# Performance work log

Measured on AMD Instinct MI355X. Metric: run time of the kernel, lower is better.

Reference implementation:

```python
import jax, jax.numpy as jnp
import numpy as np

D_MODEL, N_STATE, L_MAX, BATCH = 512, 64, 2048, 8


def _make_dplr_hippo(n):
    # HiPPO-LegS -> NPLR -> DPLR (Annotated-S4 construction)
    p0 = np.sqrt(1.0 + 2.0 * np.arange(n))
    A = p0[:, None] * p0[None, :]
    A = -(np.tril(A) - np.diag(np.arange(n)))
    p = np.sqrt(np.arange(n) + 0.5)
    S = A + p[:, None] * p[None, :]          # normal part (skew-symmetric + const diag)
    lam_re = np.mean(np.diagonal(S)) * np.ones(n)
    lam_im, V = np.linalg.eigh(S * (-1j))
    p_rot = V.conj().T @ p
    return (lam_re.astype(np.float32), lam_im.astype(np.float32),
            p_rot.real.astype(np.float32), p_rot.imag.astype(np.float32))


def setup_inputs() -> dict:
    key = jax.random.key(0)
    k = jax.random.split(key, 8)
    lam_re, lam_im, p_re, p_im = _make_dplr_hippo(N_STATE)
    dt_min, dt_max = 1e-3, 1e-1
    log_step = (jax.random.uniform(k[0], (D_MODEL,))
                * (np.log(dt_max) - np.log(dt_min)) + np.log(dt_min)).astype(jnp.float32)
    s = 0.5 ** 0.5
    B_re = jax.random.normal(k[1], (D_MODEL, N_STATE), dtype=jnp.float32) * s
    B_im = jax.random.normal(k[2], (D_MODEL, N_STATE), dtype=jnp.float32) * s
    Ct_re = jax.random.normal(k[3], (D_MODEL, N_STATE), dtype=jnp.float32) * s
    Ct_im = jax.random.normal(k[4], (D_MODEL, N_STATE), dtype=jnp.float32) * s
    D = jnp.ones((D_MODEL,), jnp.float32)
    lim = 1.0 / np.sqrt(D_MODEL)
    W = jax.random.uniform(k[5], (D_MODEL, D_MODEL), minval=-lim, maxval=lim, dtype=jnp.float32)
    b = jax.random.uniform(k[6], (D_MODEL,), minval=-lim, maxval=lim, dtype=jnp.float32)
    u = jax.random.normal(k[7], (BATCH, L_MAX, D_MODEL), dtype=jnp.float32)
    return dict(u=u,
                lam_re=jnp.asarray(lam_re), lam_im=jnp.asarray(lam_im),
                p_re=jnp.asarray(p_re), p_im=jnp.asarray(p_im),
                B_re=B_re, B_im=B_im, Ct_re=Ct_re, Ct_im=Ct_im,
                log_step=log_step, D=D, W=W, b=b,
                ln_w=jnp.ones((D_MODEL,), jnp.float32),
                ln_b=jnp.zeros((D_MODEL,), jnp.float32))


def _s4_kernel(lam, p, Bc, Ct, step, L):
    # lam, p: (n,) complex; Bc, Ct: (H, n) complex; step: (H,)
    omega = jnp.exp((-2j * jnp.pi) * (jnp.arange(L) / L))          # (L,) roots of unity
    g = (2.0 / step[:, None]) * ((1.0 - omega) / (1.0 + omega))    # (H, L) bilinear transform
    c = 2.0 / (1.0 + omega)                                        # (L,)
    cauchy = 1.0 / (g[:, :, None] - lam)                           # (H, L, n)
    a0, a1 = Ct.conj(), jnp.conj(p)[None, :]
    b0, b1 = Bc, p[None, :]
    k00 = jnp.einsum('hn,hln->hl', a0 * b0, cauchy)
    k01 = jnp.einsum('hn,hln->hl', a0 * b1, cauchy)
    k10 = jnp.einsum('hn,hln->hl', a1 * b0, cauchy)
    k11 = jnp.einsum('hn,hln->hl', a1 * b1, cauchy)
    at_roots = c * (k00 - k01 * (1.0 / (1.0 + k11)) * k10)         # generating fn at roots
    return jnp.fft.ifft(at_roots, n=L, axis=-1).real               # (H, L) real SSM kernel


def reference(u, lam_re, lam_im, p_re, p_im, B_re, B_im, Ct_re, Ct_im,
              log_step, D, W, b, ln_w, ln_b):
    L = u.shape[1]
    lam = lam_re + 1j * lam_im
    p = p_re + 1j * p_im
    Bc = B_re + 1j * B_im
    Ct = Ct_re + 1j * Ct_im
    K = _s4_kernel(lam, p, Bc, Ct, jnp.exp(log_step), L)           # (H, L)
    # causal (non-circular) convolution via zero-padded FFT
    nfft = 2 * L
    Kf = jnp.fft.rfft(K, n=nfft, axis=-1)                          # (H, L+1)
    Uf = jnp.fft.rfft(u, n=nfft, axis=1)                           # (B, L+1, H)
    y = jnp.fft.irfft(Uf * Kf.T[None], n=nfft, axis=1)[:, :L]      # (B, L, H)
    y = y + D * u                                                  # skip connection
    z = jax.nn.gelu(y, approximate=False)                          # GELU (dropout p=0)
    z = jnp.einsum('blh,oh->blo', z, W) + b                        # Linear(d_model, d_model)
    r = z + u                                                      # residual
    mean = r.mean(-1, keepdims=True)
    var = r.var(-1, keepdims=True)
    return (r - mean) / jnp.sqrt(var + 1e-5) * ln_w + ln_b         # LayerNorm
```

## Files before the change

### kernel.cpp

```cpp
#include <hip/hip_runtime.h>
#include <hip/hip_bf16.h>
#include <math.h>

#define PI_F 3.14159265358979f

typedef __attribute__((ext_vector_type(8))) short bf16x8;
typedef __attribute__((ext_vector_type(4))) float f32x4;
typedef __attribute__((ext_vector_type(2))) float f32x2;

#define DM 512
#define LSEQ 2048
#define NB 8
#define NFFT 4096
#define MTOK (NB*LSEQ)

__device__ __forceinline__ float frcp(float x) { return __builtin_amdgcn_rcpf(x); }

__device__ __forceinline__ float gelu_fast(float y) {
  float t = 0.79788456f * (y + 0.044715f * y * y * y);
  float e = __expf(2.0f * t);
  float th = 1.0f - 2.0f * frcp(e + 1.0f);
  return 0.5f * y * (1.0f + th);
}

__device__ __forceinline__ int PD(int i) { return i + (i >> 5); }
#define LDSN 4224

template<bool INV>
__device__ __forceinline__ void dft8(const float xr[8], const float xi[8],
                                     float yr[8], float yi[8]) {
  const float C = 0.70710678118654752f;
  float t0r=xr[0]+xr[4], t0i=xi[0]+xi[4];
  float t1r=xr[0]-xr[4], t1i=xi[0]-xi[4];
  float t2r=xr[2]+xr[6], t2i=xi[2]+xi[6];
  float t3r=xr[2]-xr[6], t3i=xi[2]-xi[6];
  float it3r = INV ? -t3i : t3i;
  float it3i = INV ?  t3r : -t3r;
  float E0r=t0r+t2r, E0i=t0i+t2i;
  float E2r=t0r-t2r, E2i=t0i-t2i;
  float E1r=t1r+it3r, E1i=t1i+it3i;
  float E3r=t1r-it3r, E3i=t1i-it3i;
  float u0r=xr[1]+xr[5], u0i=xi[1]+xi[5];
  float u1r=xr[1]-xr[5], u1i=xi[1]-xi[5];
  float u2r=xr[3]+xr[7], u2i=xi[3]+xi[7];
  float u3r=xr[3]-xr[7], u3i=xi[3]-xi[7];
  float iu3r = INV ? -u3i : u3i;
  float iu3i = INV ?  u3r : -u3r;
  float O0r=u0r+u2r, O0i=u0i+u2i;
  float O2r=u0r-u2r, O2i=u0i-u2i;
  float O1r=u1r+iu3r, O1i=u1i+iu3i;
  float O3r=u1r-iu3r, O3i=u1i-iu3i;
  float w1r = INV ? C*(O1r-O1i) : C*(O1r+O1i);
  float w1i = INV ? C*(O1r+O1i) : C*(O1i-O1r);
  float w2r = INV ? -O2i : O2i;
  float w2i = INV ?  O2r : -O2r;
  float w3r = INV ? -C*(O3r+O3i) : C*(O3i-O3r);
  float w3i = INV ?  C*(O3r-O3i) : -C*(O3r+O3i);
  yr[0]=E0r+O0r; yi[0]=E0i+O0i;
  yr[4]=E0r-O0r; yi[4]=E0i-O0i;
  yr[1]=E1r+w1r; yi[1]=E1i+w1i;
  yr[5]=E1r-w1r; yi[5]=E1i-w1i;
  yr[2]=E2r+w2r; yi[2]=E2i+w2i;
  yr[6]=E2r-w2r; yi[6]=E2i-w2i;
  yr[3]=E3r+w3r; yi[3]=E3i+w3i;
  yr[7]=E3r-w3r; yi[7]=E3i-w3i;
}

template<bool INV>
__device__ __forceinline__ void dft16(const float xr[16], const float xi[16],
                                      float yr[16], float yi[16]) {
  float exr[8], exi[8], oxr[8], oxi[8];
  #pragma unroll
  for (int m = 0; m < 8; ++m) {
    exr[m]=xr[2*m];   exi[m]=xi[2*m];
    oxr[m]=xr[2*m+1]; oxi[m]=xi[2*m+1];
  }
  float er[8], ei[8], orr[8], oii[8];
  dft8<INV>(exr, exi, er, ei);
  dft8<INV>(oxr, oxi, orr, oii);
  const float KC = 0.92387953251128675f;
  const float KS = 0.38268343236508977f;
  const float KH = 0.70710678118654752f;
  float tr, ti;
  yr[0]=er[0]+orr[0]; yi[0]=ei[0]+oii[0];
  yr[8]=er[0]-orr[0]; yi[8]=ei[0]-oii[0];
  { float a=KC, b=INV?KS:-KS;
    tr=orr[1]*a-oii[1]*b; ti=orr[1]*b+oii[1]*a;
    yr[1]=er[1]+tr; yi[1]=ei[1]+ti; yr[9]=er[1]-tr; yi[9]=ei[1]-ti; }
  { float a=KH, b=INV?KH:-KH;
    tr=orr[2]*a-oii[2]*b; ti=orr[2]*b+oii[2]*a;
    yr[2]=er[2]+tr; yi[2]=ei[2]+ti; yr[10]=er[2]-tr; yi[10]=ei[2]-ti; }
  { float a=KS, b=INV?KC:-KC;
    tr=orr[3]*a-oii[3]*b; ti=orr[3]*b+oii[3]*a;
    yr[3]=er[3]+tr; yi[3]=ei[3]+ti; yr[11]=er[3]-tr; yi[11]=ei[3]-ti; }
  { if (INV) { tr=-oii[4]; ti= orr[4]; } else { tr= oii[4]; ti=-orr[4]; }
    yr[4]=er[4]+tr; yi[4]=ei[4]+ti; yr[12]=er[4]-tr; yi[12]=ei[4]-ti; }
  { float a=-KS, b=INV?KC:-KC;
    tr=orr[5]*a-oii[5]*b; ti=orr[5]*b+oii[5]*a;
    yr[5]=er[5]+tr; yi[5]=ei[5]+ti; yr[13]=er[5]-tr; yi[13]=ei[5]-ti; }
  { float a=-KH, b=INV?KH:-KH;
    tr=orr[6]*a-oii[6]*b; ti=orr[6]*b+oii[6]*a;
    yr[6]=er[6]+tr; yi[6]=ei[6]+ti; yr[14]=er[6]-tr; yi[14]=ei[6]-ti; }
  { float a=-KC, b=INV?KS:-KS;
    tr=orr[7]*a-oii[7]*b; ti=orr[7]*b+oii[7]*a;
    yr[7]=er[7]+tr; yi[7]=ei[7]+ti; yr[15]=er[7]-tr; yi[15]=ei[7]-ti; }
}

template<bool INV, int NSLOG, int NBF>
__device__ __forceinline__ void r16s(float* sr, float* si, int tid,
                                     float c1, float s1f) {
  float yr[16], yi[16];
  bool act = (NBF >= 256) || (tid < NBF);
  __syncthreads();
  if (act) {
    float xr[16], xi[16];
    #pragma unroll
    for (int m = 0; m < 16; ++m) {
      int ix = PD(tid + m * NBF);
      xr[m] = sr[ix]; xi[m] = si[ix];
    }
    if (NSLOG > 0) {
      float s1 = INV ? -s1f : s1f;
      float wr = c1, wi = s1;
      #pragma unroll
      for (int m = 1; m < 16; ++m) {
        float tr = xr[m]*wr - xi[m]*wi;
        float ti = xr[m]*wi + xi[m]*wr;
        xr[m] = tr; xi[m] = ti;
        float nr = wr*c1 - wi*s1;
        float ni = wr*s1 + wi*c1;
        wr = nr; wi = ni;
      }
    }
    dft16<INV>(xr, xi, yr, yi);
  }
  __syncthreads();
  if (act) {
    int r = tid & ((1 << NSLOG) - 1);
    int q = tid >> NSLOG;
    int base = (q << (NSLOG + 4)) + r;
    #pragma unroll
    for (int p = 0; p < 16; ++p) {
      int ix = PD(base + (p << NSLOG));
      sr[ix] = yr[p]; si[ix] = yi[p];
    }
  }
}

__device__ __forceinline__ void r16s_zfirst(float* sr, float* si, int tid) {
  const float KC = 0.92387953251128675f;
  const float KS = 0.38268343236508977f;
  const float KH = 0.70710678118654752f;
  float xr[8], xi[8];
  __syncthreads();
  #pragma unroll
  for (int m = 0; m < 8; ++m) {
    int ix = PD(tid + m * 256);
    xr[m] = sr[ix]; xi[m] = si[ix];
  }
  float er[8], ei[8];
  dft8<false>(xr, xi, er, ei);
  float tr[8], ti[8];
  tr[0] = xr[0];                      ti[0] = xi[0];
  tr[1] =  xr[1]*KC + xi[1]*KS;       ti[1] =  xi[1]*KC - xr[1]*KS;
  tr[2] = (xr[2] + xi[2])*KH;         ti[2] = (xi[2] - xr[2])*KH;
  tr[3] =  xr[3]*KS + xi[3]*KC;       ti[3] =  xi[3]*KS - xr[3]*KC;
  tr[4] =  xi[4];                     ti[4] = -xr[4];
  tr[5] = -xr[5]*KS + xi[5]*KC;       ti[5] = -xi[5]*KS - xr[5]*KC;
  tr[6] = (xi[6] - xr[6])*KH;         ti[6] = -(xr[6] + xi[6])*KH;
  tr[7] = -xr[7]*KC + xi[7]*KS;       ti[7] = -xi[7]*KC - xr[7]*KS;
  float odr[8], odi[8];
  dft8<false>(tr, ti, odr, odi);
  __syncthreads();
  int base = tid << 4;
  #pragma unroll
  for (int j = 0; j < 8; ++j) {
    int ie = PD(base + 2*j), io = PD(base + 2*j + 1);
    sr[ie] = er[j];  si[ie] = ei[j];
    sr[io] = odr[j]; si[io] = odi[j];
  }
}

template<bool INV, int NSLOG, int NBF>
__device__ __forceinline__ void r8s(float* sr, float* si, int tid,
                                    float c1, float s1f) {
  float yr[8], yi[8];
  bool act = (NBF >= 256) || (tid < NBF);
  __syncthreads();
  if (act) {
    float xr[8], xi[8];
    #pragma unroll
    for (int m = 0; m < 8; ++m) {
      int ix = PD(tid + m * NBF);
      xr[m] = sr[ix]; xi[m] = si[ix];
    }
    if (NSLOG > 0) {
      float s1 = INV ? -s1f : s1f;
      float wr = c1, wi = s1;
      #pragma unroll
      for (int m = 1; m < 8; ++m) {
        float tr = xr[m]*wr - xi[m]*wi;
        float ti = xr[m]*wi + xi[m]*wr;
        xr[m] = tr; xi[m] = ti;
        float nr = wr*c1 - wi*s1;
        float ni = wr*s1 + wi*c1;
        wr = nr; wi = ni;
      }
    }
    dft8<INV>(xr, xi, yr, yi);
  }
  __syncthreads();
  if (act) {
    int r = tid & ((1 << NSLOG) - 1);
    int q = tid >> NSLOG;
    int base = (q << (NSLOG + 3)) + r;
    #pragma unroll
    for (int p = 0; p < 8; ++p) {
      int ix = PD(base + (p << NSLOG));
      sr[ix] = yr[p]; si[ix] = yi[p];
    }
  }
}

template<bool INV>
__device__ __forceinline__ void fft4096(float* sr, float* si, int tid,
                                        float cA, float sA, float cB, float sB) {
  r16s<INV, 0, 256>(sr, si, tid, 1.f, 0.f);
  r16s<INV, 4, 256>(sr, si, tid, cA, sA);
  r16s<INV, 8, 256>(sr, si, tid, cB, sB);
  __syncthreads();
}

__device__ __forceinline__ void fft4096z(float* sr, float* si, int tid,
                                         float cA, float sA, float cB, float sB) {
  r16s_zfirst(sr, si, tid);
  r16s<false, 4, 256>(sr, si, tid, cA, sA);
  r16s<false, 8, 256>(sr, si, tid, cB, sB);
  __syncthreads();
}

template<bool INV>
__device__ __forceinline__ void fft2048(float* sr, float* si, int tid,
                                        float cA, float sA, float cB, float sB) {
  r8s <INV, 0, 256>(sr, si, tid, 1.f, 0.f);
  r16s<INV, 3, 128>(sr, si, tid, cA, sA);
  r16s<INV, 7, 128>(sr, si, tid, cB, sB);
  __syncthreads();
}

__global__ __launch_bounds__(256) void k_prep(
    const float* __restrict__ lam_re, const float* __restrict__ lam_im,
    const float* __restrict__ p_re,   const float* __restrict__ p_im,
    const float* __restrict__ B_re,   const float* __restrict__ B_im,
    const float* __restrict__ Ct_re,  const float* __restrict__ Ct_im,
    float* __restrict__ wtab) {
  int idx = blockIdx.x * 256 + threadIdx.x;
  int n = idx & 63;
  float br = B_re[idx],  bi = B_im[idx];
  float cr = Ct_re[idx], ci = Ct_im[idx];
  float pr = p_re[n],    pi = p_im[n];
  float* w = wtab + (size_t)idx * 12;
  w[0] = cr*br + ci*bi;   w[1] = cr*bi - ci*br;
  w[2] = cr*pr + ci*pi;   w[3] = cr*pi - ci*pr;
  w[4] = pr*br + pi*bi;   w[5] = pr*bi - pi*br;
  w[6] = pr*pr + pi*pi;   w[7] = lam_re[n];
  w[8] = lam_im[n];       w[9] = 0.f; w[10] = 0.f; w[11] = 0.f;
}

__global__ __launch_bounds__(256) void k_mega(
    const float* __restrict__ wtab, const float* __restrict__ log_step,
    float2* __restrict__ atr,
    const float* __restrict__ u, float* __restrict__ ut,
    const float* __restrict__ W, __hip_bfloat16* __restrict__ Wb) {
  __shared__ float tsh[32][33];
  int bidx = blockIdx.x;
  int tid = threadIdx.x;
  if (bidx < 2048) {
    int h = bidx >> 2;
    int l0 = ((bidx & 3) << 8) + tid;
    int l1 = l0 + 1024;
    float two_over_step = 2.0f * expf(-log_step[h]);
    float omi0, omr0, omi1, omr1;
    sincosf(-2.0f * PI_F * (float)l0 / (float)LSEQ, &omi0, &omr0);
    sincosf(-2.0f * PI_F * (float)l1 / (float)LSEQ, &omi1, &omr1);
    float a0 = 1.0f + omr0, a1 = 1.0f + omr1;
    float iv0 = frcp(a0*a0 + omi0*omi0);
    float iv1 = frcp(a1*a1 + omi1*omi1);
    float cr0 = 2.0f*a0*iv0, ci0 = -2.0f*omi0*iv0;
    float cr1 = 2.0f*a1*iv1, ci1 = -2.0f*omi1*iv1;
    f32x2 gr, gi;
    gr.x = two_over_step * (1.0f - omr0*omr0 - omi0*omi0) * iv0;
    gr.y = two_over_step * (1.0f - omr1*omr1 - omi1*omi1) * iv1;
    gi.x = two_over_step * (-2.0f * omi0) * iv0;
    gi.y = two_over_step * (-2.0f * omi1) * iv1;
    f32x2 K00r={0.f,0.f},K00i={0.f,0.f},K01r={0.f,0.f},K01i={0.f,0.f},
          K10r={0.f,0.f},K10i={0.f,0.f},K11r={0.f,0.f},K11i={0.f,0.f};
    const float4* wq = (const float4*)(wtab + (size_t)h * 64 * 12);
    #pragma unroll 8
    for (int n = 0; n < 64; ++n) {
      float4 wa = wq[n*3+0];
      float4 wb = wq[n*3+1];
      float  lim = wq[n*3+2].x;
      f32x2 dr = gr - wb.w;
      f32x2 di = gi - lim;
      f32x2 den = dr*dr + di*di;
      f32x2 inv; inv.x = frcp(den.x); inv.y = frcp(den.y);
      f32x2 car = dr*inv, cai = -di*inv;
      K00r += wa.x*car - wa.y*cai;  K00i += wa.x*cai + wa.y*car;
      K01r += wa.z*car - wa.w*cai;  K01i += wa.z*cai + wa.w*car;
      K10r += wb.x*car - wb.y*cai;  K10i += wb.x*cai + wb.y*car;
      K11r += wb.z*car;             K11i += wb.z*cai;
    }
    {
      float tr = K01r.x*K10r.x - K01i.x*K10i.x, ti = K01r.x*K10i.x + K01i.x*K10r.x;
      float d1r = 1.0f + K11r.x, d1i = K11i.x;
      float invd1 = frcp(d1r*d1r + d1i*d1i);
      float t2r = (tr*d1r + ti*d1i) * invd1;
      float t2i = (ti*d1r - tr*d1i) * invd1;
      float numr = K00r.x - t2r, numi = K00i.x - t2i;
      atr[(size_t)h * LSEQ + l0] = make_float2(cr0*numr - ci0*numi, cr0*numi + ci0*numr);
    }
    {
      float tr = K01r.y*K10r.y - K01i.y*K10i.y, ti = K01r.y*K10i.y + K01i.y*K10r.y;
      float d1r = 1.0f + K11r.y, d1i = K11i.y;
      float invd1 = frcp(d1r*d1r + d1i*d1i);
      float t2r = (tr*d1r + ti*d1i) * invd1;
      float t2i = (ti*d1r - tr*d1i) * invd1;
      float numr = K00r.y - t2r, numi = K00i.y - t2i;
      atr[(size_t)h * LSEQ + l1] = make_float2(cr1*numr - ci1*numi, cr1*numi + ci1*numr);
    }
  } else if (bidx < 2048 + 8192) {
    int t = bidx - 2048;
    int lx = t & 63, hy = (t >> 6) & 15, b = t >> 10;
    int l0 = lx * 32, h0 = hy * 32;
    int x = tid & 31, y0 = tid >> 5;
    #pragma unroll
    for (int i = 0; i < 4; ++i) {
      int y = y0 + i*8;
      tsh[y][x] = u[((size_t)b*LSEQ + l0 + y) * DM + h0 + x];
    }
    __syncthreads();
    #pragma unroll
    for (int i = 0; i < 4; ++i) {
      int y = y0 + i*8;
      ut[((size_t)b*DM + h0 + y) * LSEQ + l0 + x] = tsh[x][y];
    }
  } else {
    int i = (bidx - 10240) * 256 + tid;
    Wb[i] = __float2bfloat16(W[i]);
  }
}

__global__ __launch_bounds__(256, 4) void k_fftK(const float2* __restrict__ atr,
                                                 float2* __restrict__ Kf) {
  __shared__ float sr[LDSN], si[LDSN];
  int h = blockIdx.x, tid = threadIdx.x;
  float c2a, s2a, c2b, s2b, c4a, s4a, c4b, s4b;
  { int r = tid & 7;   __sincosf(-2.f*PI_F*(float)r/128.f,  &s2a, &c2a); }
  { int r = tid & 127; __sincosf(-2.f*PI_F*(float)r/2048.f, &s2b, &c2b); }
  { int r = tid & 15;  __sincosf(-2.f*PI_F*(float)r/256.f,  &s4a, &c4a); }
  { int r = tid;       __sincosf(-2.f*PI_F*(float)r/4096.f, &s4b, &c4b); }
  const float2* ap = atr + (size_t)h * LSEQ;
  #pragma unroll
  for (int i = 0; i < 8; ++i) {
    int l = tid + i*256;
    float2 v = ap[l];
    sr[PD(l)] = v.x; si[PD(l)] = v.y;
  }
  fft2048<true>(sr, si, tid, c2a, s2a, c2b, s2b);
  #pragma unroll
  for (int i = 0; i < 8; ++i) {
    int m = tid + i*256;
    float v = sr[PD(m)] * (1.0f / (float)LSEQ);
    sr[PD(m)] = v;
    si[PD(m)] = 0.0f;
  }
  fft4096z(sr, si, tid, c4a, s4a, c4b, s4b);
  float2* ko = Kf + (size_t)h * NFFT;
  #pragma unroll
  for (int i = 0; i < 16; ++i) {
    int f = tid + i*256;
    ko[f] = make_float2(sr[PD(f)], si[PD(f)]);
  }
}

__global__ __launch_bounds__(256, 4) void k_conv(const float* __restrict__ ut,
                                                 const float2* __restrict__ Kf,
                                                 const float* __restrict__ Dvec,
                                                 __hip_bfloat16* __restrict__ zbt) {
  __shared__ float sr[LDSN], si[LDSN];
  int wg = blockIdx.x;
  int bp = wg >> 9, h = wg & 511;
  int b0 = bp*2, b1 = bp*2 + 1;
  int tid = threadIdx.x;
  float c4a, s4a, c4b, s4b;
  { int r = tid & 15; __sincosf(-2.f*PI_F*(float)r/256.f,  &s4a, &c4a); }
  { int r = tid;      __sincosf(-2.f*PI_F*(float)r/4096.f, &s4b, &c4b); }
  const float* u0p = ut + ((size_t)(b0*DM + h)) * LSEQ;
  const float* u1p = ut + ((size_t)(b1*DM + h)) * LSEQ;
  #pragma unroll
  for (int i = 0; i < 8; ++i) {
    int l = tid + i*256;
    sr[PD(l)] = u0p[l];  si[PD(l)] = u1p[l];
  }
  fft4096z(sr, si, tid, c4a, s4a, c4b, s4b);
  float yrg[16], yig[16];
  const float2* kp = Kf + (size_t)h * NFFT;
  #pragma unroll
  for (int i = 0; i < 16; ++i) {
    int f = tid + i*256;
    int fn = (NFFT - f) & (NFFT - 1);
    float ar = sr[PD(f)],  ai = si[PD(f)];
    float br = sr[PD(fn)], bi = -si[PD(fn)];
    float u0r = 0.5f*(ar + br), u0i = 0.5f*(ai + bi);
    float u1r = 0.5f*(ai - bi), u1i = -0.5f*(ar - br);
    float2 K0 = kp[f];
    float y0r = u0r*K0.x - u0i*K0.y, y0i = u0r*K0.y + u0i*K0.x;
    float y1r = u1r*K0.x - u1i*K0.y, y1i = u1r*K0.y + u1i*K0.x;
    yrg[i] = y0r - y1i;
    yig[i] = y0i + y1r;
  }
  __syncthreads();
  #pragma unroll
  for (int i = 0; i < 16; ++i) {
    int f = tid + i*256;
    sr[PD(f)] = yrg[i]; si[PD(f)] = yig[i];
  }
  fft4096<true>(sr, si, tid, c4a, s4a, c4b, s4b);
  float d = Dvec[h];
  __hip_bfloat16* zb0 = zbt + ((size_t)(b0*DM + h)) * LSEQ;
  __hip_bfloat16* zb1 = zbt + ((size_t)(b1*DM + h)) * LSEQ;
  const float inv_n = 1.0f / (float)NFFT;
  #pragma unroll
  for (int i = 0; i < 8; ++i) {
    int l = tid + i*256;
    float y0 = sr[PD(l)]*inv_n + d*u0p[l];
    float y1 = si[PD(l)]*inv_n + d*u1p[l];
    zb0[l] = __float2bfloat16(gelu_fast(y0));
    zb1[l] = __float2bfloat16(gelu_fast(y1));
  }
}

__global__ __launch_bounds__(512) void k_gemm_ln(
    const ushort* __restrict__ zbt,
    const short* __restrict__ Wb,
    const float* __restrict__ bias,
    const float* __restrict__ u,
    const float* __restrict__ lnw, const float* __restrict__ lnb,
    float* __restrict__ out) {
  __shared__ ushort sA[64][40];
  __shared__ short sB[512][40];
  __shared__ float red[2][4][64];
  __shared__ float smu[64], srs[64];
  __shared__ float sln[2][DM];
  int tid = threadIdx.x, wave = tid >> 6, lane = tid & 63;
  int wm = wave >> 2, wn = wave & 3;
  int m0 = blockIdx.x * 64;
  int b = m0 >> 11;
  int l0 = m0 & (LSEQ - 1);
  const ushort* zb = zbt + (size_t)b * DM * LSEQ;
  int row = lane & 15, kq8 = (lane >> 4) << 3;
  int kk = tid >> 4, seg = tid & 15;
  int cB = (tid & 3) << 3, rB = tid >> 2;
  sln[0][tid] = lnw[tid];
  sln[1][tid] = lnb[tid];
  f32x4 acc[2][8];
  #pragma unroll
  for (int i = 0; i < 2; ++i)
    #pragma unroll
    for (int j = 0; j < 8; ++j) acc[i][j] = (f32x4){0.f,0.f,0.f,0.f};
  for (int k0 = 0; k0 < DM; k0 += 32) {
    __syncthreads();
    {
      uint2 v = *(const uint2*)(zb + (size_t)(k0 + kk)*LSEQ + l0 + seg*4);
      const ushort* p = (const ushort*)&v;
      sA[seg*4 + 0][kk] = p[0];
      sA[seg*4 + 1][kk] = p[1];
      sA[seg*4 + 2][kk] = p[2];
      sA[seg*4 + 3][kk] = p[3];
    }
    #pragma unroll
    for (int jj = 0; jj < 4; ++jj) {
      int o = rB + jj*128;
      *(uint4*)&sB[o][cB] = *(const uint4*)(Wb + (size_t)o*DM + k0 + cB);
    }
    __syncthreads();
    bf16x8 a0 = *(const bf16x8*)&sA[wm*32 + row][kq8];
    bf16x8 a1 = *(const bf16x8*)&sA[wm*32 + 16 + row][kq8];
    #pragma unroll
    for (int nt = 0; nt < 8; ++nt) {
      bf16x8 bf = *(const bf16x8*)&sB[wn*128 + nt*16 + row][kq8];
      acc[0][nt] = __builtin_amdgcn_mfma_f32_16x16x32_bf16(a0, bf, acc[0][nt], 0, 0, 0);
      acc[1][nt] = __builtin_amdgcn_mfma_f32_16x16x32_bf16(a1, bf, acc[1][nt], 0, 0, 0);
    }
  }
  int ccol = lane & 15, crow = (lane >> 4) << 2;
  #pragma unroll
  for (int rt = 0; rt < 2; ++rt) {
    #pragma unroll
    for (int rr = 0; rr < 4; ++rr) {
      int lr = wm*32 + rt*16 + crow + rr;
      int gr = m0 + lr;
      float ls = 0.f, ls2 = 0.f;
      #pragma unroll
      for (int nt = 0; nt < 8; ++nt) {
        int col = wn*128 + nt*16 + ccol;
        float v = acc[rt][nt][rr] + bias[col] + u[(size_t)gr*DM + col];
        acc[rt][nt][rr] = v;
        ls += v; ls2 += v*v;
      }
      ls  += __shfl_xor(ls, 1);  ls2 += __shfl_xor(ls2, 1);
      ls  += __shfl_xor(ls, 2);  ls2 += __shfl_xor(ls2, 2);
      ls  += __shfl_xor(ls, 4);  ls2 += __shfl_xor(ls2, 4);
      ls  += __shfl_xor(ls, 8);  ls2 += __shfl_xor(ls2, 8);
      if (ccol == 0) { red[0][wn][lr] = ls; red[1][wn][lr] = ls2; }
    }
  }
  __syncthreads();
  if (tid < 64) {
    float s = red[0][0][tid] + red[0][1][tid] + red[0][2][tid] + red[0][3][tid];
    float q = red[1][0][tid] + red[1][1][tid] + red[1][2][tid] + red[1][3][tid];
    float mean = s * (1.0f/(float)DM);
    float var  = q * (1.0f/(float)DM) - mean*mean;
    smu[tid] = mean;
    srs[tid] = rsqrtf(var + 1e-5f);
  }
  __syncthreads();
  #pragma unroll
  for (int rt = 0; rt < 2; ++rt) {
    #pragma unroll
    for (int rr = 0; rr < 4; ++rr) {
      int lr = wm*32 + rt*16 + crow + rr;
      int gr = m0 + lr;
      float mu = smu[lr], rs = srs[lr];
      #pragma unroll
      for (int nt = 0; nt < 8; ++nt) {
        int col = wn*128 + nt*16 + ccol;
        out[(size_t)gr*DM + col] = (acc[rt][nt][rr] - mu) * rs * sln[0][col] + sln[1][col];
      }
    }
  }
}

extern "C" void kernel_launch(void* const* d_in, const int* in_sizes, int n_in,
                              void* d_out, int out_size, void* d_ws, size_t ws_size,
                              hipStream_t stream) {
  const float* u        = (const float*)d_in[0];
  const float* lam_re   = (const float*)d_in[1];
  const float* lam_im   = (const float*)d_in[2];
  const float* p_re     = (const float*)d_in[3];
  const float* p_im     = (const float*)d_in[4];
  const float* B_re     = (const float*)d_in[5];
  const float* B_im     = (const float*)d_in[6];
  const float* Ct_re    = (const float*)d_in[7];
  const float* Ct_im    = (const float*)d_in[8];
  const float* log_step = (const float*)d_in[9];
  const float* Dv       = (const float*)d_in[10];
  const float* W        = (const float*)d_in[11];
  const float* bias     = (const float*)d_in[12];
  const float* ln_w     = (const float*)d_in[13];
  const float* ln_b     = (const float*)d_in[14];
  float* out = (float*)d_out;
  char* ws = (char*)d_ws;

  float2* Kf = (float2*)ws;
  float*  ut = (float*)(ws + (16u << 20));
  __hip_bfloat16* zbt = (__hip_bfloat16*)(ws + (48u << 20));
  float2* atr  = (float2*)(ws + (48u << 20));
  float*  wtab = (float*)(ws + (56u << 20));
  __hip_bfloat16* Wb = (__hip_bfloat16*)(ws + (64u << 20));
  if (ws_size < (65u << 20)) return;

  k_prep<<<dim3(128), dim3(256), 0, stream>>>(lam_re, lam_im, p_re, p_im,
                                              B_re, B_im, Ct_re, Ct_im, wtab);
  k_mega<<<dim3(2048 + 8192 + 1024), dim3(256), 0, stream>>>(
      wtab, log_step, atr, u, ut, W, Wb);
  k_fftK<<<dim3(DM), dim3(256), 0, stream>>>(atr, Kf);
  k_conv<<<dim3((NB/2) * DM), dim3(256), 0, stream>>>(ut, Kf, Dv, zbt);
  k_gemm_ln<<<dim3(MTOK/64), dim3(512), 0, stream>>>((const ushort*)zbt, (const short*)Wb,
                                                     bias, u, ln_w, ln_b, out);
}
```

Baseline: 125.7 us.

## Precompute FFT twiddle powers and bilinear omega table; pair reciprocals in kernel gen

The convolution kernel now precomputes the 15 twiddle powers per radix-16 stage once per thread and reuses them across the forward and inverse FFTs, replacing the per-stage recurrence. The prep kernel also builds a table of bilinear-transform factors per frequency, so the kernel-generation blocks load them instead of calling sincosf. The inner Cauchy loop replaces two reciprocals with one shared reciprocal of the product. The costs are higher register pressure from 60 extra twiddle registers under launch bounds of 4 blocks, and a possible loss of precision or overflow from the paired reciprocal.

```diff
diff --git a/kernel.cpp b/kernel.cpp
--- a/kernel.cpp
+++ b/kernel.cpp
@@ -147,6 +147,53 @@
   }
 }
 
+template<bool INV, int NSLOG>
+__device__ __forceinline__ void r16s_tw(float* sr, float* si, int tid,
+                                        const float* twr, const float* twi) {
+  float yr[16], yi[16];
+  __syncthreads();
+  {
+    float xr[16], xi[16];
+    #pragma unroll
+    for (int m = 0; m < 16; ++m) {
+      int ix = PD(tid + m * 256);
+      xr[m] = sr[ix]; xi[m] = si[ix];
+    }
+    if (NSLOG > 0) {
+      #pragma unroll
+      for (int m = 1; m < 16; ++m) {
+        float wr = twr[m-1];
+        float wi = INV ? -twi[m-1] : twi[m-1];
+        float tr = xr[m]*wr - xi[m]*wi;
+        float ti = xr[m]*wi + xi[m]*wr;
+        xr[m] = tr; xi[m] = ti;
+      }
+    }
+    dft16<INV>(xr, xi, yr, yi);
+  }
+  __syncthreads();
+  {
+    int r = tid & ((1 << NSLOG) - 1);
+    int q = tid >> NSLOG;
+    int base = (q << (NSLOG + 4)) + r;
+    #pragma unroll
+    for (int p = 0; p < 16; ++p) {
+      int ix = PD(base + (p << NSLOG));
+      sr[ix] = yr[p]; si[ix] = yi[p];
+    }
+  }
+}
+
+__device__ __forceinline__ void tw_powers(float c, float s,
+                                          float* twr, float* twi) {
+  twr[0] = c; twi[0] = s;
+  #pragma unroll
+  for (int m = 1; m < 15; ++m) {
+    twr[m] = twr[m-1]*c - twi[m-1]*s;
+    twi[m] = twr[m-1]*s + twi[m-1]*c;
+  }
+}
+
 __device__ __forceinline__ void r16s_zfirst(float* sr, float* si, int tid) {
   const float KC = 0.92387953251128675f;
   const float KS = 0.38268343236508977f;
@@ -223,11 +270,19 @@
 }
 
 template<bool INV>
-__device__ __forceinline__ void fft4096(float* sr, float* si, int tid,
-                                        float cA, float sA, float cB, float sB) {
-  r16s<INV, 0, 256>(sr, si, tid, 1.f, 0.f);
-  r16s<INV, 4, 256>(sr, si, tid, cA, sA);
-  r16s<INV, 8, 256>(sr, si, tid, cB, sB);
+__device__ __forceinline__ void fft4096t(float* sr, float* si, int tid,
+    const float* twAr, const float* twAi, const float* twBr, const float* twBi) {
+  r16s_tw<INV, 0>(sr, si, tid, twAr, twAi);
+  r16s_tw<INV, 4>(sr, si, tid, twAr, twAi);
+  r16s_tw<INV, 8>(sr, si, tid, twBr, twBi);
+  __syncthreads();
+}
+
+__device__ __forceinline__ void fft4096tz(float* sr, float* si, int tid,
+    const float* twAr, const float* twAi, const float* twBr, const float* twBi) {
+  r16s_zfirst(sr, si, tid);
+  r16s_tw<false, 4>(sr, si, tid, twAr, twAi);
+  r16s_tw<false, 8>(sr, si, tid, twBr, twBi);
   __syncthreads();
 }
 
@@ -253,23 +308,38 @@
     const float* __restrict__ p_re,   const float* __restrict__ p_im,
     const float* __restrict__ B_re,   const float* __restrict__ B_im,
     const float* __restrict__ Ct_re,  const float* __restrict__ Ct_im,
-    float* __restrict__ wtab) {
-  int idx = blockIdx.x * 256 + threadIdx.x;
-  int n = idx & 63;
-  float br = B_re[idx],  bi = B_im[idx];
-  float cr = Ct_re[idx], ci = Ct_im[idx];
-  float pr = p_re[n],    pi = p_im[n];
-  float* w = wtab + (size_t)idx * 12;
-  w[0] = cr*br + ci*bi;   w[1] = cr*bi - ci*br;
-  w[2] = cr*pr + ci*pi;   w[3] = cr*pi - ci*pr;
-  w[4] = pr*br + pi*bi;   w[5] = pr*bi - pi*br;
-  w[6] = pr*pr + pi*pi;   w[7] = lam_re[n];
-  w[8] = lam_im[n];       w[9] = 0.f; w[10] = 0.f; w[11] = 0.f;
+    float* __restrict__ wtab, float4* __restrict__ otab) {
+  int bidx = blockIdx.x;
+  if (bidx < 128) {
+    int idx = bidx * 256 + threadIdx.x;
+    int n = idx & 63;
+    float br = B_re[idx],  bi = B_im[idx];
+    float cr = Ct_re[idx], ci = Ct_im[idx];
+    float pr = p_re[n],    pi = p_im[n];
+    float* w = wtab + (size_t)idx * 12;
+    w[0] = cr*br + ci*bi;   w[1] = cr*bi - ci*br;
+    w[2] = cr*pr + ci*pi;   w[3] = cr*pi - ci*pr;
+    w[4] = pr*br + pi*bi;   w[5] = pr*bi - pi*br;
+    w[6] = pr*pr + pi*pi;   w[7] = lam_re[n];
+    w[8] = lam_im[n];       w[9] = 0.f; w[10] = 0.f; w[11] = 0.f;
+  } else {
+    int l = (bidx - 128) * 256 + threadIdx.x;
+    float omi, omr;
+    sincosf(-2.0f * PI_F * (float)l / (float)LSEQ, &omi, &omr);
+    float a = 1.0f + omr;
+    float iv = frcp(a*a + omi*omi);
+    float4 o;
+    o.x = 2.0f * a * iv;
+    o.y = -2.0f * omi * iv;
+    o.z = (1.0f - omr*omr - omi*omi) * iv;
+    o.w = (-2.0f * omi) * iv;
+    otab[l] = o;
+  }
 }
 
 __global__ __launch_bounds__(256) void k_mega(
-    const float* __restrict__ wtab, const float* __restrict__ log_step,
-    float2* __restrict__ atr,
+    const float* __restrict__ wtab, const float4* __restrict__ otab,
+    const float* __restrict__ log_step, float2* __restrict__ atr,
     const float* __restrict__ u, float* __restrict__ ut,
     const float* __restrict__ W, __hip_bfloat16* __restrict__ Wb) {
   __shared__ float tsh[32][33];
@@ -279,20 +349,13 @@
     int h = bidx >> 2;
     int l0 = ((bidx & 3) << 8) + tid;
     int l1 = l0 + 1024;
-    float two_over_step = 2.0f * expf(-log_step[h]);
-    float omi0, omr0, omi1, omr1;
-    sincosf(-2.0f * PI_F * (float)l0 / (float)LSEQ, &omi0, &omr0);
-    sincosf(-2.0f * PI_F * (float)l1 / (float)LSEQ, &omi1, &omr1);
-    float a0 = 1.0f + omr0, a1 = 1.0f + omr1;
-    float iv0 = frcp(a0*a0 + omi0*omi0);
-    float iv1 = frcp(a1*a1 + omi1*omi1);
-    float cr0 = 2.0f*a0*iv0, ci0 = -2.0f*omi0*iv0;
-    float cr1 = 2.0f*a1*iv1, ci1 = -2.0f*omi1*iv1;
+    float tos = 2.0f * expf(-log_step[h]);
+    float4 o0 = otab[l0];
+    float4 o1 = otab[l1];
+    float cr0 = o0.x, ci0 = o0.y, cr1 = o1.x, ci1 = o1.y;
     f32x2 gr, gi;
-    gr.x = two_over_step * (1.0f - omr0*omr0 - omi0*omi0) * iv0;
-    gr.y = two_over_step * (1.0f - omr1*omr1 - omi1*omi1) * iv1;
-    gi.x = two_over_step * (-2.0f * omi0) * iv0;
-    gi.y = two_over_step * (-2.0f * omi1) * iv1;
+    gr.x = tos * o0.z;  gr.y = tos * o1.z;
+    gi.x = tos * o0.w;  gi.y = tos * o1.w;
     f32x2 K00r={0.f,0.f},K00i={0.f,0.f},K01r={0.f,0.f},K01i={0.f,0.f},
           K10r={0.f,0.f},K10i={0.f,0.f},K11r={0.f,0.f},K11i={0.f,0.f};
     const float4* wq = (const float4*)(wtab + (size_t)h * 64 * 12);
@@ -304,7 +367,8 @@
       f32x2 dr = gr - wb.w;
       f32x2 di = gi - lim;
       f32x2 den = dr*dr + di*di;
-      f32x2 inv; inv.x = frcp(den.x); inv.y = frcp(den.y);
+      float ip = frcp(den.x * den.y);
+      f32x2 inv; inv.x = den.y * ip; inv.y = den.x * ip;
       f32x2 car = dr*inv, cai = -di*inv;
       K00r += wa.x*car - wa.y*cai;  K00i += wa.x*cai + wa.y*car;
       K01r += wa.z*car - wa.w*cai;  K01i += wa.z*cai + wa.w*car;
@@ -396,6 +460,9 @@
   float c4a, s4a, c4b, s4b;
   { int r = tid & 15; __sincosf(-2.f*PI_F*(float)r/256.f,  &s4a, &c4a); }
   { int r = tid;      __sincosf(-2.f*PI_F*(float)r/4096.f, &s4b, &c4b); }
+  float twAr[15], twAi[15], twBr[15], twBi[15];
+  tw_powers(c4a, s4a, twAr, twAi);
+  tw_powers(c4b, s4b, twBr, twBi);
   const float* u0p = ut + ((size_t)(b0*DM + h)) * LSEQ;
   const float* u1p = ut + ((size_t)(b1*DM + h)) * LSEQ;
   #pragma unroll
@@ -403,7 +470,7 @@
     int l = tid + i*256;
     sr[PD(l)] = u0p[l];  si[PD(l)] = u1p[l];
   }
-  fft4096z(sr, si, tid, c4a, s4a, c4b, s4b);
+  fft4096tz(sr, si, tid, twAr, twAi, twBr, twBi);
   float yrg[16], yig[16];
   const float2* kp = Kf + (size_t)h * NFFT;
   #pragma unroll
@@ -426,7 +493,7 @@
     int f = tid + i*256;
     sr[PD(f)] = yrg[i]; si[PD(f)] = yig[i];
   }
-  fft4096<true>(sr, si, tid, c4a, s4a, c4b, s4b);
+  fft4096t<true>(sr, si, tid, twAr, twAi, twBr, twBi);
   float d = Dvec[h];
   __hip_bfloat16* zb0 = zbt + ((size_t)(b0*DM + h)) * LSEQ;
   __hip_bfloat16* zb1 = zbt + ((size_t)(b1*DM + h)) * LSEQ;
@@ -568,13 +635,14 @@
   __hip_bfloat16* zbt = (__hip_bfloat16*)(ws + (48u << 20));
   float2* atr  = (float2*)(ws + (48u << 20));
   float*  wtab = (float*)(ws + (56u << 20));
+  float4* otab = (float4*)(ws + (58u << 20));
   __hip_bfloat16* Wb = (__hip_bfloat16*)(ws + (64u << 20));
   if (ws_size < (65u << 20)) return;
 
-  k_prep<<<dim3(128), dim3(256), 0, stream>>>(lam_re, lam_im, p_re, p_im,
-                                              B_re, B_im, Ct_re, Ct_im, wtab);
+  k_prep<<<dim3(136), dim3(256), 0, stream>>>(lam_re, lam_im, p_re, p_im,
+                                              B_re, B_im, Ct_re, Ct_im, wtab, otab);
   k_mega<<<dim3(2048 + 8192 + 1024), dim3(256), 0, stream>>>(
-      wtab, log_step, atr, u, ut, W, Wb);
+      wtab, otab, log_step, atr, u, ut, W, Wb);
   k_fftK<<<dim3(DM), dim3(256), 0, stream>>>(atr, Kf);
   k_conv<<<dim3((NB/2) * DM), dim3(256), 0, stream>>>(ut, Kf, Dv, zbt);
   k_gemm_ln<<<dim3(MTOK/64), dim3(512), 0, stream>>>((const ushort*)zbt, (const short*)Wb,
```

After: 163.3 us. 29.9% more time.
